# Performance work log

Measured on AMD Instinct MI355X. Metric: run time of the kernel, lower is better.

The kernel has to match this reference:

```python
import jax, jax.numpy as jnp
import numpy as np

HEAD = 4
EPS = 1e-12


def _l2norm(x, axis):
    # torch F.normalize: x / max(||x||_2, eps)
    return x / jnp.maximum(jnp.linalg.norm(x, axis=axis, keepdims=True), EPS)


def setup_inputs() -> dict:
    key = jax.random.key(0)
    ks = jax.random.split(key, 12)
    n, t, c, h, w = 2, 7, 96, 96, 96
    inp = {
        "curr_feat": jax.random.normal(ks[0], (n, c, h, w), jnp.float32),
        "index_feat_set_s1": jax.random.normal(ks[1], (n, t, c, h, w), jnp.float32),
        "anchor_feat": jax.random.normal(ks[2], (n, c, h, w), jnp.float32),
        "sparse_feat_set_s1": jax.random.normal(ks[3], (n, t, c, h, w), jnp.float32),
        "sparse_feat_set_s2": jax.random.normal(ks[4], (n, t, c, h, w), jnp.float32),
        "sparse_feat_set_s3": jax.random.normal(ks[5], (n, t, c, h, w), jnp.float32),
        # absolute pixel coordinates (x,y interleaved per frame), mostly in-bounds
        # with a little overshoot to exercise zeros padding of grid_sample
        "location_feat": jax.random.uniform(ks[6], (n, t * 2, h, w), jnp.float32, minval=-2.0, maxval=float(w) + 1.0),
        "proj_w": 0.02 * jax.random.normal(ks[7], (c, c), jnp.float32),
        "proj_b": jnp.zeros((c,), jnp.float32),
        "fusion_w": 0.02 * jax.random.normal(ks[8], (c, 3 * c), jnp.float32),
        "fusion_b": jnp.zeros((c,), jnp.float32),
    }
    return inp


def reference(curr_feat, index_feat_set_s1, anchor_feat, sparse_feat_set_s1,
              sparse_feat_set_s2, sparse_feat_set_s3, location_feat,
              proj_w, proj_b, fusion_w, fusion_b):
    n, c, h, w = anchor_feat.shape
    t = sparse_feat_set_s1.shape[1]
    hd = c // HEAD
    hw = h * w

    # ---- flow-guided nearest grid_sample (align_corners=True, zeros pad) ----
    loc = location_feat.reshape(n, t, 2, h, w)  # (n,t,2,h,w): [x, y] pixel coords
    gx = 2.0 * loc[:, :, 0] / max(w - 1, 1) - 1.0
    gy = 2.0 * loc[:, :, 1] / max(h - 1, 1) - 1.0
    ix = jnp.round((gx + 1.0) * 0.5 * (w - 1))  # nearest (round-half-even, as torch)
    iy = jnp.round((gy + 1.0) * 0.5 * (h - 1))
    valid = (ix >= 0) & (ix <= w - 1) & (iy >= 0) & (iy <= h - 1)
    lin = (jnp.clip(iy, 0, h - 1).astype(jnp.int32) * w
           + jnp.clip(ix, 0, w - 1).astype(jnp.int32)).reshape(n, t, 1, hw)
    vmask = valid.reshape(n, t, 1, hw)

    def sample(f):  # f: (n,t,c,h,w) -> gathered (n,t,c,hw)
        g = jnp.take_along_axis(f.reshape(n, t, c, hw), lin, axis=3)
        return jnp.where(vmask, g, 0.0)

    samp1 = sample(sparse_feat_set_s1)
    samp2 = sample(sparse_feat_set_s2)
    samp3 = sample(sparse_feat_set_s3)
    sampi = sample(index_feat_set_s1)

    # ---- per-pixel multi-head max-correlation over t frames ----
    # queries: normalize over full channel dim c BEFORE splitting into heads
    q = _l2norm(curr_feat.reshape(n, c, hw).transpose(0, 2, 1), -1).reshape(n, hw, HEAD, hd)
    k = _l2norm(sampi.transpose(0, 3, 1, 2), -1).reshape(n, hw, t, HEAD, hd)
    scores = jnp.einsum('npthd,nphd->npht', k, q)  # scale == 1.0 in mode='max'
    corr_soft = jnp.max(scores, axis=3)     # (n,hw,head)
    corr_index = jnp.argmax(scores, axis=3)  # (n,hw,head), first-max like torch

    soft_img = jnp.broadcast_to(corr_soft[..., None], (n, hw, HEAD, hd)) \
                  .reshape(n, h, w, c).transpose(0, 3, 1, 2)  # (n,c,h,w)
    idx = jnp.broadcast_to(corr_index[..., None], (n, hw, HEAD, hd)) \
             .reshape(n, hw, c).transpose(0, 2, 1)[:, None]  # (n,1,c,hw)

    def pick(samp):  # select winning frame per (channel-group, pixel)
        return jnp.take_along_axis(samp, idx, axis=1)[:, 0].reshape(n, c, h, w)

    cat = jnp.concatenate([pick(samp1), pick(samp2), pick(samp3)], axis=1)  # (n,3c,h,w)
    out = jnp.einsum('ndhw,cd->nchw', cat, fusion_w) + fusion_b[None, :, None, None]
    out = out * soft_img
    out = jnp.einsum('nchw,dc->ndhw', out, proj_w) + proj_b[None, :, None, None]
    return out + anchor_feat
```

## Files before the change

kernel.cpp:

```cpp
#include <hip/hip_runtime.h>
#include <hip/hip_bf16.h>

#define N_    2
#define T_    7
#define C_    96
#define H_    96
#define W_    96
#define HW_   9216
#define HEAD_ 4
#define HD_   24
#define C3_   288
#define P_    16
#define QP_   100
#define CATP_ 292
#define NBLK_ (N_ * (HW_ / P_))
#define PLANES_ 14
#define CHUNK_  64
#define NCHUNK_ 144

typedef unsigned int u32;

__device__ __forceinline__ float bits2f(u32 b) {
    union { u32 u; float f; } x; x.u = b; return x.f;
}

__device__ __forceinline__ unsigned short f2bf(float f) {
    union { __hip_bfloat16 h; unsigned short s; } u;
    u.h = __float2bfloat16(f);
    return u.s;
}

template<bool BF16>
__device__ __forceinline__ float ld1(const void* p, int i) {
    if constexpr (BF16) return bits2f(((u32)((const unsigned short*)p)[i]) << 16);
    else                return ((const float*)p)[i];
}

template<bool BF16>
__device__ __forceinline__ void ld4w(const void* p, int i, float w[4]) {
    if constexpr (BF16) {
        const uint2 u = ((const uint2*)p)[i >> 2];
        w[0] = bits2f(u.x << 16);
        w[1] = bits2f(u.x & 0xFFFF0000u);
        w[2] = bits2f(u.y << 16);
        w[3] = bits2f(u.y & 0xFFFF0000u);
    } else {
        const float4 v = *((const float4*)((const float*)p + i));
        w[0] = v.x; w[1] = v.y; w[2] = v.z; w[3] = v.w;
    }
}

template<bool BF16>
__device__ __forceinline__ void st1(void* p, int i, float v) {
    if constexpr (BF16) ((unsigned short*)p)[i] = f2bf(v);
    else                ((float*)p)[i] = v;
}

template<bool BF16>
__device__ __forceinline__ void st4w(void* p, int i, const float v[4]) {
    if constexpr (BF16) {
        uint2 w;
        w.x = (u32)f2bf(v[0]) | ((u32)f2bf(v[1]) << 16);
        w.y = (u32)f2bf(v[2]) | ((u32)f2bf(v[3]) << 16);
        ((uint2*)p)[i >> 2] = w;
    } else {
        *((float4*)((float*)p + i)) = make_float4(v[0], v[1], v[2], v[3]);
    }
}

__device__ __forceinline__ bool block_detect_bf16(const u32* __restrict__ w,
                                                  int tid, int* s_flag) {
    if (tid < 64) {
        u32 x = w[tid];
        u32 f = x & 0x7FFFu;
        int inwin = (f >= 0x3A00u) && (f <= 0x4200u);
        unsigned long long m = __ballot(inwin);
        if (tid == 0) *s_flag = (__popcll(m) >= 40) ? 1 : 0;
    }
    __syncthreads();
    return *s_flag != 0;
}

template<bool BF16>
__device__ __forceinline__ void transp_body(const void* __restrict__ src,
                                            void* __restrict__ dst,
                                            int bx, int tid, char* tileraw) {
    const int pl = bx / NCHUNK_;
    const int x0 = (bx - pl * NCHUNK_) * CHUNK_;
    if constexpr (BF16) {
        unsigned short (*tile)[CHUNK_ + 2] = (unsigned short (*)[CHUNK_ + 2])tileraw;
        const unsigned short* s = (const unsigned short*)src;
        unsigned short* d = (unsigned short*)dst;
        for (int i = tid; i < C_ * (CHUNK_ / 4); i += 256) {
            int ch = i >> 4, xq = i & 15;
            const ushort4 v = *((const ushort4*)(s + (pl * C_ + ch) * HW_ + x0 + 4 * xq));
            tile[ch][4 * xq + 0] = v.x; tile[ch][4 * xq + 1] = v.y;
            tile[ch][4 * xq + 2] = v.z; tile[ch][4 * xq + 3] = v.w;
        }
        __syncthreads();
        for (int i = tid; i < CHUNK_ * (C_ / 4); i += 256) {
            int p = i / 24, cq = i - p * 24;
            ushort4 v;
            v.x = tile[4 * cq + 0][p]; v.y = tile[4 * cq + 1][p];
            v.z = tile[4 * cq + 2][p]; v.w = tile[4 * cq + 3][p];
            *((ushort4*)(d + (pl * HW_ + x0 + p) * C_ + 4 * cq)) = v;
        }
    } else {
        float (*tile)[CHUNK_ + 1] = (float (*)[CHUNK_ + 1])tileraw;
        const float* s = (const float*)src;
        float* d = (float*)dst;
        for (int i = tid; i < C_ * (CHUNK_ / 4); i += 256) {
            int ch = i >> 4, xq = i & 15;
            const float4 v = *((const float4*)(s + (pl * C_ + ch) * HW_ + x0 + 4 * xq));
            tile[ch][4 * xq + 0] = v.x; tile[ch][4 * xq + 1] = v.y;
            tile[ch][4 * xq + 2] = v.z; tile[ch][4 * xq + 3] = v.w;
        }
        __syncthreads();
        for (int i = tid; i < CHUNK_ * (C_ / 4); i += 256) {
            int p = i / 24, cq = i - p * 24;
            float4 v;
            v.x = tile[4 * cq + 0][p]; v.y = tile[4 * cq + 1][p];
            v.z = tile[4 * cq + 2][p]; v.w = tile[4 * cq + 3][p];
            *((float4*)(d + (pl * HW_ + x0 + p) * C_ + 4 * cq)) = v;
        }
    }
}

__global__ __launch_bounds__(256) void transp_kernel(
    const void* __restrict__ idxf, void* __restrict__ dst,
    const u32* __restrict__ detect_src)
{
    __shared__ __align__(16) char tileraw[C_ * (CHUNK_ + 1) * 4];
    __shared__ int s_flag;
    const int tid = threadIdx.x;
    const bool bf = block_detect_bf16(detect_src, tid, &s_flag);
    if (bf) transp_body<true >(idxf, dst, blockIdx.x, tid, tileraw);
    else    transp_body<false>(idxf, dst, blockIdx.x, tid, tileraw);
}

template<bool BF16>
__device__ __forceinline__ void argmax_body(
    const void* __restrict__ curr, const void* __restrict__ loc,
    const void* __restrict__ kT,
    float* __restrict__ ws_best, int* __restrict__ ws_gbase,
    float* s_u, int (*s_lin)[P_], float (*s_red)[8],
    float (*s_best)[HEAD_], int (*s_bidx)[HEAD_], float* s_inv)
{
#define S_Q(pp, ch)  s_u[(pp) * QP_ + (ch)]
#define S_K(pp, ch)  s_u[P_ * QP_ + (pp) * QP_ + (ch)]
    const int tid = threadIdx.x;
    const int b  = blockIdx.x;
    const int nn = b / (HW_ / P_);
    const int p0 = (b - nn * (HW_ / P_)) * P_;

    if (tid < T_ * P_) {
        int t = tid / P_, pp = tid - t * P_;
        int p = p0 + pp;
        float x = ld1<BF16>(loc, (nn * 2 * T_ + 2 * t    ) * HW_ + p);
        float y = ld1<BF16>(loc, (nn * 2 * T_ + 2 * t + 1) * HW_ + p);
        float gx = 2.0f * x / 95.0f - 1.0f;
        float gy = 2.0f * y / 95.0f - 1.0f;
        float fx = (gx + 1.0f) * 0.5f * 95.0f;
        float fy = (gy + 1.0f) * 0.5f * 95.0f;
        float ix = rintf(fx), iy = rintf(fy);
        bool v = (ix >= 0.0f) && (ix <= 95.0f) && (iy >= 0.0f) && (iy <= 95.0f);
        s_lin[t][pp] = v ? ((int)iy * W_ + (int)ix) : -1;
    }
    if (tid >= 128 && tid < 128 + P_ * HEAD_) {
        int q = tid - 128;
        s_best[q >> 2][q & 3] = -3.0e38f; s_bidx[q >> 2][q & 3] = 0;
    }

    for (int i = tid; i < C_ * (P_ / 4); i += 256) {
        int ch = i >> 2, pq = i & 3;
        float w[4];
        ld4w<BF16>(curr, (nn * C_ + ch) * HW_ + p0 + 4 * pq, w);
        S_Q(4 * pq + 0, ch) = w[0]; S_Q(4 * pq + 1, ch) = w[1];
        S_Q(4 * pq + 2, ch) = w[2]; S_Q(4 * pq + 3, ch) = w[3];
    }
    __syncthreads();

    if (tid < P_ * 8) {
        int pp = tid >> 3, j = tid & 7;
        float s = 0.f;
        #pragma unroll
        for (int k = 0; k < 12; ++k) { float v = S_Q(pp, j * 12 + k); s += v * v; }
        s_red[pp][j] = s;
    }
    __syncthreads();
    if (tid < P_) {
        float s = 0.f;
        #pragma unroll
        for (int j = 0; j < 8; ++j) s += s_red[tid][j];
        s_inv[tid] = 1.0f / fmaxf(sqrtf(s), 1e-12f);
    }
    __syncthreads();
    for (int i = tid; i < C_ * P_; i += 256) {
        int pp = i & (P_ - 1), ch = i >> 4;
        S_Q(pp, ch) *= s_inv[pp];
    }

    for (int t = 0; t < T_; ++t) {
        __syncthreads();
        for (int i = tid; i < 24 * P_; i += 256) {
            int pp = i / 24, j = i - pp * 24;
            int lin = s_lin[t][pp];
            float w[4] = {0.f, 0.f, 0.f, 0.f};
            if (lin >= 0) ld4w<BF16>(kT, ((nn * T_ + t) * HW_ + lin) * C_ + 4 * j, w);
            *((float4*)&S_K(pp, 4 * j)) = make_float4(w[0], w[1], w[2], w[3]);
        }
        __syncthreads();
        if (tid < P_ * 8) {
            int pp = tid >> 3, j = tid & 7;
            float s = 0.f;
            #pragma unroll
            for (int k = 0; k < 12; ++k) { float v = S_K(pp, j * 12 + k); s += v * v; }
            s_red[pp][j] = s;
        }
        __syncthreads();
        if (tid < P_) {
            float s = 0.f;
            #pragma unroll
            for (int j = 0; j < 8; ++j) s += s_red[tid][j];
            s_inv[tid] = 1.0f / fmaxf(sqrtf(s), 1e-12f);
        }
        __syncthreads();
        if (tid < P_ * HEAD_) {
            int pp = tid >> 2, h = tid & 3;
            float s = 0.f;
            #pragma unroll
            for (int dq = 0; dq < 6; ++dq) {
                const float4 kv = *((const float4*)&S_K(pp, h * HD_ + 4 * dq));
                const float4 qv = *((const float4*)&S_Q(pp, h * HD_ + 4 * dq));
                s += kv.x * qv.x; s += kv.y * qv.y; s += kv.z * qv.z; s += kv.w * qv.w;
            }
            s *= s_inv[pp];
            if (s > s_best[pp][h]) { s_best[pp][h] = s; s_bidx[pp][h] = t; }
        }
    }
    if (tid < P_ * HEAD_) {
        int pp = tid >> 2, h = tid & 3;
        int bt = s_bidx[pp][h];
        int lin = s_lin[bt][pp];
        int g = (nn * HW_ + p0 + pp) * HEAD_ + h;
        ws_best[g]  = s_best[pp][h];
        ws_gbase[g] = (lin >= 0) ? ((nn * T_ + bt) * C_ * HW_ + lin) : -1;
    }
#undef S_Q
#undef S_K
}

__global__ __launch_bounds__(256, 8) void argmax_kernel(
    const void* __restrict__ curr, const void* __restrict__ loc,
    const void* __restrict__ kT,
    float* __restrict__ ws_best, int* __restrict__ ws_gbase)
{
    __shared__ __align__(16) float s_u[2 * P_ * QP_];
    __shared__ int   s_lin[T_][P_];
    __shared__ float s_red[P_][8];
    __shared__ float s_best[P_][HEAD_];
    __shared__ int   s_bidx[P_][HEAD_];
    __shared__ float s_inv[P_];
    __shared__ int   s_flag;
    const bool bf = block_detect_bf16((const u32*)curr, threadIdx.x, &s_flag);
    if (bf) argmax_body<true >(curr, loc, kT, ws_best, ws_gbase, s_u, s_lin, s_red, s_best, s_bidx, s_inv);
    else    argmax_body<false>(curr, loc, kT, ws_best, ws_gbase, s_u, s_lin, s_red, s_best, s_bidx, s_inv);
}

template<bool BF16>
__device__ __forceinline__ void catgemv_body(
    const void* __restrict__ anchor, const void* __restrict__ s1,
    const void* __restrict__ s2, const void* __restrict__ s3,
    const void* __restrict__ pw, const void* __restrict__ pb,
    const void* __restrict__ fw, const void* __restrict__ fb,
    void* __restrict__ outp,
    const float* __restrict__ ws_best, const int* __restrict__ ws_gbase,
    float* s_u, float (*s_mid)[QP_], float (*s_best)[HEAD_], int (*s_gbase)[HEAD_])
{
#define S_CAT(pp, d) s_u[(pp) * CATP_ + (d)]
    const int tid = threadIdx.x;
    const int b  = blockIdx.x;
    const int nn = b / (HW_ / P_);
    const int p0 = (b - nn * (HW_ / P_)) * P_;

    if (tid < P_ * HEAD_) {
        int pp = tid >> 2, h = tid & 3;
        int g = (nn * HW_ + p0 + pp) * HEAD_ + h;
        s_best[pp][h]  = ws_best[g];
        s_gbase[pp][h] = ws_gbase[g];
    }
    __syncthreads();

    for (int i = tid; i < C3_ * P_; i += 256) {
        int pp = i / C3_, d = i - pp * C3_;
        int set = d / C_, ch = d - set * C_;
        int gb = s_gbase[pp][ch / HD_];
        float v = 0.f;
        if (gb >= 0) {
            const void* sp = (set == 0) ? s1 : (set == 1) ? s2 : s3;
            v = ld1<BF16>(sp, gb + ch * HW_);
        }
        S_CAT(pp, d) = v;
    }
    __syncthreads();

    if (tid < 192) {
        const int cp = tid >> 2, pq = tid & 3;
        const int co0 = cp * 2, px0 = pq * 4;
        float acc[2][4];
        #pragma unroll
        for (int r = 0; r < 2; ++r)
            #pragma unroll
            for (int k = 0; k < 4; ++k) acc[r][k] = 0.f;
        for (int d = 0; d < C3_; d += 4) {
            float4 cv[4];
            #pragma unroll
            for (int k = 0; k < 4; ++k) cv[k] = *((const float4*)&S_CAT(px0 + k, d));
            #pragma unroll
            for (int r = 0; r < 2; ++r) {
                float w[4]; ld4w<BF16>(fw, (co0 + r) * C3_ + d, w);
                #pragma unroll
                for (int k = 0; k < 4; ++k)
                    acc[r][k] += w[0] * cv[k].x + w[1] * cv[k].y + w[2] * cv[k].z + w[3] * cv[k].w;
            }
        }
        const int hh = co0 / HD_;
        #pragma unroll
        for (int r = 0; r < 2; ++r) {
            float fbv = ld1<BF16>(fb, co0 + r);
            #pragma unroll
            for (int k = 0; k < 4; ++k)
                s_mid[px0 + k][co0 + r] = (acc[r][k] + fbv) * s_best[px0 + k][hh];
        }
    }
    __syncthreads();

    if (tid < 192) {
        const int dp = tid >> 2, pq = tid & 3;
        const int do0 = dp * 2, px0 = pq * 4;
        float acc[2][4];
        #pragma unroll
        for (int r = 0; r < 2; ++r)
            #pragma unroll
            for (int k = 0; k < 4; ++k) acc[r][k] = 0.f;
        for (int c = 0; c < C_; c += 4) {
            float4 mv[4];
            #pragma unroll
            for (int k = 0; k < 4; ++k) mv[k] = *((const float4*)&s_mid[px0 + k][c]);
            #pragma unroll
            for (int r = 0; r < 2; ++r) {
                float w[4]; ld4w<BF16>(pw, (do0 + r) * C_ + c, w);
                #pragma unroll
                for (int k = 0; k < 4; ++k)
                    acc[r][k] += w[0] * mv[k].x + w[1] * mv[k].y + w[2] * mv[k].z + w[3] * mv[k].w;
            }
        }
        #pragma unroll
        for (int r = 0; r < 2; ++r) {
            float pbv = ld1<BF16>(pb, do0 + r);
            float av[4];
            ld4w<BF16>(anchor, (nn * C_ + do0 + r) * HW_ + p0 + px0, av);
            float res[4];
            #pragma unroll
            for (int k = 0; k < 4; ++k) res[k] = acc[r][k] + pbv + av[k];
            st4w<BF16>(outp, (nn * C_ + do0 + r) * HW_ + p0 + px0, res);
        }
    }
#undef S_CAT
}

__global__ __launch_bounds__(256, 6) void catgemv_kernel(
    const void* __restrict__ curr, const void* __restrict__ anchor,
    const void* __restrict__ s1, const void* __restrict__ s2,
    const void* __restrict__ s3, const void* __restrict__ pw,
    const void* __restrict__ pb, const void* __restrict__ fw,
    const void* __restrict__ fb, void* __restrict__ outp,
    const float* __restrict__ ws_best, const int* __restrict__ ws_gbase)
{
    __shared__ __align__(16) float s_u[P_ * CATP_];
    __shared__ __align__(16) float s_mid[P_][QP_];
    __shared__ float s_best[P_][HEAD_];
    __shared__ int   s_gbase[P_][HEAD_];
    __shared__ int   s_flag;
    const bool bf = block_detect_bf16((const u32*)curr, threadIdx.x, &s_flag);
    if (bf) catgemv_body<true >(anchor, s1, s2, s3, pw, pb, fw, fb, outp, ws_best, ws_gbase,
                                s_u, s_mid, s_best, s_gbase);
    else    catgemv_body<false>(anchor, s1, s2, s3, pw, pb, fw, fb, outp, ws_best, ws_gbase,
                                s_u, s_mid, s_best, s_gbase);
}

template<bool BF16>
__device__ __forceinline__ void mono_body(
    const void* __restrict__ curr, const void* __restrict__ idxf,
    const void* __restrict__ anchor, const void* __restrict__ s1,
    const void* __restrict__ s2, const void* __restrict__ s3,
    const void* __restrict__ loc, const void* __restrict__ pw,
    const void* __restrict__ pb, const void* __restrict__ fw,
    const void* __restrict__ fb, void* __restrict__ outp,
    float* s_u, float (*s_mid)[QP_], int (*s_lin)[P_], float (*s_red)[8],
    float (*s_best)[HEAD_], int (*s_bidx)[HEAD_], float* s_inv)
{
#define S_Q(pp, ch)  s_u[(pp) * QP_ + (ch)]
#define S_K(pp, ch)  s_u[P_ * QP_ + (pp) * QP_ + (ch)]
#define S_CAT(pp, d) s_u[(pp) * CATP_ + (d)]
    const int tid = threadIdx.x;
    const int b  = blockIdx.x;
    const int nn = b / (HW_ / P_);
    const int p0 = (b - nn * (HW_ / P_)) * P_;

    if (tid < T_ * P_) {
        int t = tid / P_, pp = tid - t * P_;
        int p = p0 + pp;
        float x = ld1<BF16>(loc, (nn * 2 * T_ + 2 * t    ) * HW_ + p);
        float y = ld1<BF16>(loc, (nn * 2 * T_ + 2 * t + 1) * HW_ + p);
        float gx = 2.0f * x / 95.0f - 1.0f;
        float gy = 2.0f * y / 95.0f - 1.0f;
        float fx = (gx + 1.0f) * 0.5f * 95.0f;
        float fy = (gy + 1.0f) * 0.5f * 95.0f;
        float ix = rintf(fx), iy = rintf(fy);
        bool v = (ix >= 0.0f) && (ix <= 95.0f) && (iy >= 0.0f) && (iy <= 95.0f);
        s_lin[t][pp] = v ? ((int)iy * W_ + (int)ix) : -1;
    }
    if (tid >= 128 && tid < 128 + P_ * HEAD_) {
        int q = tid - 128;
        s_best[q >> 2][q & 3] = -3.0e38f; s_bidx[q >> 2][q & 3] = 0;
    }
    for (int i = tid; i < C_ * (P_ / 4); i += 256) {
        int ch = i >> 2, pq = i & 3;
        float w[4];
        ld4w<BF16>(curr, (nn * C_ + ch) * HW_ + p0 + 4 * pq, w);
        S_Q(4 * pq + 0, ch) = w[0]; S_Q(4 * pq + 1, ch) = w[1];
        S_Q(4 * pq + 2, ch) = w[2]; S_Q(4 * pq + 3, ch) = w[3];
    }
    __syncthreads();
    if (tid < P_ * 8) {
        int pp = tid >> 3, j = tid & 7;
        float s = 0.f;
        #pragma unroll
        for (int k = 0; k < 12; ++k) { float v = S_Q(pp, j * 12 + k); s += v * v; }
        s_red[pp][j] = s;
    }
    __syncthreads();
    if (tid < P_) {
        float s = 0.f;
        #pragma unroll
        for (int j = 0; j < 8; ++j) s += s_red[tid][j];
        s_inv[tid] = 1.0f / fmaxf(sqrtf(s), 1e-12f);
    }
    __syncthreads();
    for (int i = tid; i < C_ * P_; i += 256) {
        int pp = i & (P_ - 1), ch = i >> 4;
        S_Q(pp, ch) *= s_inv[pp];
    }
    for (int t = 0; t < T_; ++t) {
        __syncthreads();
        for (int i = tid; i < C_ * P_; i += 256) {
            int ch = i / P_, pp = i - ch * P_;
            int lin = s_lin[t][pp];
            S_K(pp, ch) = (lin >= 0) ? ld1<BF16>(idxf, ((nn * T_ + t) * C_ + ch) * HW_ + lin) : 0.0f;
        }
        __syncthreads();
        if (tid < P_ * 8) {
            int pp = tid >> 3, j = tid & 7;
            float s = 0.f;
            #pragma unroll
            for (int k = 0; k < 12; ++k) { float v = S_K(pp, j * 12 + k); s += v * v; }
            s_red[pp][j] = s;
        }
        __syncthreads();
        if (tid < P_) {
            float s = 0.f;
            #pragma unroll
            for (int j = 0; j < 8; ++j) s += s_red[tid][j];
            s_inv[tid] = 1.0f / fmaxf(sqrtf(s), 1e-12f);
        }
        __syncthreads();
        if (tid < P_ * HEAD_) {
            int pp = tid >> 2, h = tid & 3;
            float s = 0.f;
            #pragma unroll
            for (int dq = 0; dq < 6; ++dq) {
                const float4 kv = *((const float4*)&S_K(pp, h * HD_ + 4 * dq));
                const float4 qv = *((const float4*)&S_Q(pp, h * HD_ + 4 * dq));
                s += kv.x * qv.x; s += kv.y * qv.y; s += kv.z * qv.z; s += kv.w * qv.w;
            }
            s *= s_inv[pp];
            if (s > s_best[pp][h]) { s_best[pp][h] = s; s_bidx[pp][h] = t; }
        }
    }
    __syncthreads();
    for (int i = tid; i < C3_ * P_; i += 256) {
        int pp = i / C3_, d = i - pp * C3_;
        int set = d / C_, ch = d - set * C_;
        int h = ch / HD_;
        int bt = s_bidx[pp][h];
        int lin = s_lin[bt][pp];
        float v = 0.f;
        if (lin >= 0) {
            const void* sp = (set == 0) ? s1 : (set == 1) ? s2 : s3;
            v = ld1<BF16>(sp, ((nn * T_ + bt) * C_ + ch) * HW_ + lin);
        }
        S_CAT(pp, d) = v;
    }
    __syncthreads();
    if (tid < 96) {
        const int cq = tid >> 2, pq = tid & 3;
        const int co0 = cq * 4, px0 = pq * 4;
        float acc[4][4];
        #pragma unroll
        for (int r = 0; r < 4; ++r)
            #pragma unroll
            for (int k = 0; k < 4; ++k) acc[r][k] = 0.f;
        for (int d = 0; d < C3_; d += 4) {
            float4 cv[4];
            #pragma unroll
            for (int k = 0; k < 4; ++k) cv[k] = *((const float4*)&S_CAT(px0 + k, d));
            #pragma unroll
            for (int r = 0; r < 4; ++r) {
                float w[4]; ld4w<BF16>(fw, (co0 + r) * C3_ + d, w);
                #pragma unroll
                for (int k = 0; k < 4; ++k)
                    acc[r][k] += w[0] * cv[k].x + w[1] * cv[k].y + w[2] * cv[k].z + w[3] * cv[k].w;
            }
        }
        const int hh = co0 / HD_;
        #pragma unroll
        for (int r = 0; r < 4; ++r) {
            float fbv = ld1<BF16>(fb, co0 + r);
            #pragma unroll
            for (int k = 0; k < 4; ++k)
                s_mid[px0 + k][co0 + r] = (acc[r][k] + fbv) * s_best[px0 + k][hh];
        }
    }
    __syncthreads();
    if (tid < 96) {
        const int dq = tid >> 2, pq = tid & 3;
        const int do0 = dq * 4, px0 = pq * 4;
        float acc[4][4];
        #pragma unroll
        for (int r = 0; r < 4; ++r)
            #pragma unroll
            for (int k = 0; k < 4; ++k) acc[r][k] = 0.f;
        for (int c = 0; c < C_; c += 4) {
            float4 mv[4];
            #pragma unroll
            for (int k = 0; k < 4; ++k) mv[k] = *((const float4*)&s_mid[px0 + k][c]);
            #pragma unroll
            for (int r = 0; r < 4; ++r) {
                float w[4]; ld4w<BF16>(pw, (do0 + r) * C_ + c, w);
                #pragma unroll
                for (int k = 0; k < 4; ++k)
                    acc[r][k] += w[0] * mv[k].x + w[1] * mv[k].y + w[2] * mv[k].z + w[3] * mv[k].w;
            }
        }
        #pragma unroll
        for (int r = 0; r < 4; ++r) {
            float pbv = ld1<BF16>(pb, do0 + r);
            float av[4];
            ld4w<BF16>(anchor, (nn * C_ + do0 + r) * HW_ + p0 + px0, av);
            float res[4];
            #pragma unroll
            for (int k = 0; k < 4; ++k) res[k] = acc[r][k] + pbv + av[k];
            st4w<BF16>(outp, (nn * C_ + do0 + r) * HW_ + p0 + px0, res);
        }
    }
#undef S_Q
#undef S_K
#undef S_CAT
}

__global__ __launch_bounds__(256) void mono_kernel(
    const void* __restrict__ curr, const void* __restrict__ idxf,
    const void* __restrict__ anchor, const void* __restrict__ s1,
    const void* __restrict__ s2, const void* __restrict__ s3,
    const void* __restrict__ loc, const void* __restrict__ pw,
    const void* __restrict__ pb, const void* __restrict__ fw,
    const void* __restrict__ fb, void* __restrict__ outp)
{
    __shared__ __align__(16) float s_u[P_ * CATP_];
    __shared__ __align__(16) float s_mid[P_][QP_];
    __shared__ int   s_lin[T_][P_];
    __shared__ float s_red[P_][8];
    __shared__ float s_best[P_][HEAD_];
    __shared__ int   s_bidx[P_][HEAD_];
    __shared__ float s_inv[P_];
    __shared__ int   s_flag;
    const bool bf = block_detect_bf16((const u32*)curr, threadIdx.x, &s_flag);
    if (bf) mono_body<true >(curr, idxf, anchor, s1, s2, s3, loc, pw, pb, fw, fb, outp,
                             s_u, s_mid, s_lin, s_red, s_best, s_bidx, s_inv);
    else    mono_body<false>(curr, idxf, anchor, s1, s2, s3, loc, pw, pb, fw, fb, outp,
                             s_u, s_mid, s_lin, s_red, s_best, s_bidx, s_inv);
}

extern "C" void kernel_launch(void* const* d_in, const int* in_sizes, int n_in,
                              void* d_out, int out_size, void* d_ws, size_t ws_size,
                              hipStream_t stream) {
    (void)in_sizes; (void)n_in; (void)out_size;
    const unsigned long long SZB  = (unsigned long long)N_ * T_ * HW_ * C_ * 4ull;
    const unsigned long long AUXB = (unsigned long long)N_ * HW_ * HEAD_ * 4ull;
    char* wsb = (char*)d_ws;
    void*  kT       = wsb;
    float* ws_best  = (float*)(wsb + SZB);
    int*   ws_gbase = (int*)  (wsb + SZB + AUXB);

    dim3 grid(NBLK_), block(256);
    if (ws_size >= SZB + 2 * AUXB) {
        transp_kernel<<<dim3(PLANES_ * NCHUNK_), 256, 0, stream>>>(d_in[1], kT, (const u32*)d_in[0]);
        argmax_kernel<<<grid, block, 0, stream>>>(d_in[0], d_in[6], kT, ws_best, ws_gbase);
        catgemv_kernel<<<grid, block, 0, stream>>>(d_in[0], d_in[2], d_in[3], d_in[4], d_in[5],
                                                   d_in[7], d_in[8], d_in[9], d_in[10], d_out,
                                                   ws_best, ws_gbase);
    } else {
        mono_kernel<<<grid, block, 0, stream>>>(d_in[0], d_in[1], d_in[2], d_in[3], d_in[4],
                                                d_in[5], d_in[6], d_in[7], d_in[8], d_in[9],
                                                d_in[10], d_out);
    }
}
```

Measured before the change: 323.6 us.

## Transpose sparse feature sets to channel-last for vectorized winner gather

When enough workspace is available, the transpose kernel now converts all three sparse feature sets to a pixel-major, channel-contiguous layout in addition to the index features. The argmax kernel emits gather bases for that layout, and the cat/GEMV kernel loads the winning frame's channels as float4 vectors instead of strided scalars. This removes uncoalesced per-channel gathers but adds a full read and write of three large tensors plus a larger workspace requirement.

```diff
diff --git a/kernel.cpp b/kernel.cpp
--- a/kernel.cpp
+++ b/kernel.cpp
@@ -127,18 +127,23 @@
 }
 
 __global__ __launch_bounds__(256) void transp_kernel(
-    const void* __restrict__ idxf, void* __restrict__ dst,
+    const void* __restrict__ a0, const void* __restrict__ a1,
+    const void* __restrict__ a2, const void* __restrict__ a3,
+    void* __restrict__ dstb, unsigned long long szb,
     const u32* __restrict__ detect_src)
 {
     __shared__ __align__(16) char tileraw[C_ * (CHUNK_ + 1) * 4];
     __shared__ int s_flag;
+    const int arr = blockIdx.y;
+    const void* src = (arr == 0) ? a0 : (arr == 1) ? a1 : (arr == 2) ? a2 : a3;
+    void* dst = (char*)dstb + (unsigned long long)arr * szb;
     const int tid = threadIdx.x;
     const bool bf = block_detect_bf16(detect_src, tid, &s_flag);
-    if (bf) transp_body<true >(idxf, dst, blockIdx.x, tid, tileraw);
-    else    transp_body<false>(idxf, dst, blockIdx.x, tid, tileraw);
-}
-
-template<bool BF16>
+    if (bf) transp_body<true >(src, dst, blockIdx.x, tid, tileraw);
+    else    transp_body<false>(src, dst, blockIdx.x, tid, tileraw);
+}
+
+template<bool BF16, bool TGB>
 __device__ __forceinline__ void argmax_body(
     const void* __restrict__ curr, const void* __restrict__ loc,
     const void* __restrict__ kT,
@@ -243,13 +248,18 @@
         int bt = s_bidx[pp][h];
         int lin = s_lin[bt][pp];
         int g = (nn * HW_ + p0 + pp) * HEAD_ + h;
-        ws_best[g]  = s_best[pp][h];
-        ws_gbase[g] = (lin >= 0) ? ((nn * T_ + bt) * C_ * HW_ + lin) : -1;
+        ws_best[g] = s_best[pp][h];
+        int gb;
+        if (lin < 0)       gb = -1;
+        else if (TGB)      gb = ((nn * T_ + bt) * HW_ + lin) * C_;
+        else               gb = (nn * T_ + bt) * C_ * HW_ + lin;
+        ws_gbase[g] = gb;
     }
 #undef S_Q
 #undef S_K
 }
 
+template<bool TGB>
 __global__ __launch_bounds__(256, 8) void argmax_kernel(
     const void* __restrict__ curr, const void* __restrict__ loc,
     const void* __restrict__ kT,
@@ -263,11 +273,11 @@
     __shared__ float s_inv[P_];
     __shared__ int   s_flag;
     const bool bf = block_detect_bf16((const u32*)curr, threadIdx.x, &s_flag);
-    if (bf) argmax_body<true >(curr, loc, kT, ws_best, ws_gbase, s_u, s_lin, s_red, s_best, s_bidx, s_inv);
-    else    argmax_body<false>(curr, loc, kT, ws_best, ws_gbase, s_u, s_lin, s_red, s_best, s_bidx, s_inv);
-}
-
-template<bool BF16>
+    if (bf) argmax_body<true , TGB>(curr, loc, kT, ws_best, ws_gbase, s_u, s_lin, s_red, s_best, s_bidx, s_inv);
+    else    argmax_body<false, TGB>(curr, loc, kT, ws_best, ws_gbase, s_u, s_lin, s_red, s_best, s_bidx, s_inv);
+}
+
+template<bool BF16, bool TRANS>
 __device__ __forceinline__ void catgemv_body(
     const void* __restrict__ anchor, const void* __restrict__ s1,
     const void* __restrict__ s2, const void* __restrict__ s3,
@@ -291,16 +301,30 @@
     }
     __syncthreads();
 
-    for (int i = tid; i < C3_ * P_; i += 256) {
-        int pp = i / C3_, d = i - pp * C3_;
-        int set = d / C_, ch = d - set * C_;
-        int gb = s_gbase[pp][ch / HD_];
-        float v = 0.f;
-        if (gb >= 0) {
-            const void* sp = (set == 0) ? s1 : (set == 1) ? s2 : s3;
-            v = ld1<BF16>(sp, gb + ch * HW_);
-        }
-        S_CAT(pp, d) = v;
+    if constexpr (TRANS) {
+        for (int i = tid; i < P_ * 72; i += 256) {
+            int px = i / 72, j = i - px * 72;
+            int set = j / 24, jj = j - set * 24;
+            int gb = s_gbase[px][jj / 6];
+            float w[4] = {0.f, 0.f, 0.f, 0.f};
+            if (gb >= 0) {
+                const void* sp = (set == 0) ? s1 : (set == 1) ? s2 : s3;
+                ld4w<BF16>(sp, gb + 4 * jj, w);
+            }
+            *((float4*)&S_CAT(px, set * C_ + 4 * jj)) = make_float4(w[0], w[1], w[2], w[3]);
+        }
+    } else {
+        for (int i = tid; i < C3_ * P_; i += 256) {
+            int pp = i / C3_, d = i - pp * C3_;
+            int set = d / C_, ch = d - set * C_;
+            int gb = s_gbase[pp][ch / HD_];
+            float v = 0.f;
+            if (gb >= 0) {
+                const void* sp = (set == 0) ? s1 : (set == 1) ? s2 : s3;
+                v = ld1<BF16>(sp, gb + ch * HW_);
+            }
+            S_CAT(pp, d) = v;
+        }
     }
     __syncthreads();
 
@@ -369,6 +393,7 @@
 #undef S_CAT
 }
 
+template<bool TRANS>
 __global__ __launch_bounds__(256, 6) void catgemv_kernel(
     const void* __restrict__ curr, const void* __restrict__ anchor,
     const void* __restrict__ s1, const void* __restrict__ s2,
@@ -383,10 +408,10 @@
     __shared__ int   s_gbase[P_][HEAD_];
     __shared__ int   s_flag;
     const bool bf = block_detect_bf16((const u32*)curr, threadIdx.x, &s_flag);
-    if (bf) catgemv_body<true >(anchor, s1, s2, s3, pw, pb, fw, fb, outp, ws_best, ws_gbase,
-                                s_u, s_mid, s_best, s_gbase);
-    else    catgemv_body<false>(anchor, s1, s2, s3, pw, pb, fw, fb, outp, ws_best, ws_gbase,
-                                s_u, s_mid, s_best, s_gbase);
+    if (bf) catgemv_body<true , TRANS>(anchor, s1, s2, s3, pw, pb, fw, fb, outp, ws_best, ws_gbase,
+                                       s_u, s_mid, s_best, s_gbase);
+    else    catgemv_body<false, TRANS>(anchor, s1, s2, s3, pw, pb, fw, fb, outp, ws_best, ws_gbase,
+                                       s_u, s_mid, s_best, s_gbase);
 }
 
 template<bool BF16>
@@ -599,17 +624,31 @@
     const unsigned long long SZB  = (unsigned long long)N_ * T_ * HW_ * C_ * 4ull;
     const unsigned long long AUXB = (unsigned long long)N_ * HW_ * HEAD_ * 4ull;
     char* wsb = (char*)d_ws;
-    void*  kT       = wsb;
-    float* ws_best  = (float*)(wsb + SZB);
-    int*   ws_gbase = (int*)  (wsb + SZB + AUXB);
 
     dim3 grid(NBLK_), block(256);
-    if (ws_size >= SZB + 2 * AUXB) {
-        transp_kernel<<<dim3(PLANES_ * NCHUNK_), 256, 0, stream>>>(d_in[1], kT, (const u32*)d_in[0]);
-        argmax_kernel<<<grid, block, 0, stream>>>(d_in[0], d_in[6], kT, ws_best, ws_gbase);
-        catgemv_kernel<<<grid, block, 0, stream>>>(d_in[0], d_in[2], d_in[3], d_in[4], d_in[5],
-                                                   d_in[7], d_in[8], d_in[9], d_in[10], d_out,
-                                                   ws_best, ws_gbase);
+    if (ws_size >= 4 * SZB + 2 * AUXB) {
+        void*  kT       = wsb;
+        void*  s1T      = wsb + SZB;
+        void*  s2T      = wsb + 2 * SZB;
+        void*  s3T      = wsb + 3 * SZB;
+        float* ws_best  = (float*)(wsb + 4 * SZB);
+        int*   ws_gbase = (int*)  (wsb + 4 * SZB + AUXB);
+        transp_kernel<<<dim3(PLANES_ * NCHUNK_, 4), 256, 0, stream>>>(
+            d_in[1], d_in[3], d_in[4], d_in[5], wsb, SZB, (const u32*)d_in[0]);
+        argmax_kernel<true><<<grid, block, 0, stream>>>(d_in[0], d_in[6], kT, ws_best, ws_gbase);
+        catgemv_kernel<true><<<grid, block, 0, stream>>>(d_in[0], d_in[2], s1T, s2T, s3T,
+                                                         d_in[7], d_in[8], d_in[9], d_in[10],
+                                                         d_out, ws_best, ws_gbase);
+    } else if (ws_size >= SZB + 2 * AUXB) {
+        void*  kT       = wsb;
+        float* ws_best  = (float*)(wsb + SZB);
+        int*   ws_gbase = (int*)  (wsb + SZB + AUXB);
+        transp_kernel<<<dim3(PLANES_ * NCHUNK_, 1), 256, 0, stream>>>(
+            d_in[1], d_in[1], d_in[1], d_in[1], wsb, SZB, (const u32*)d_in[0]);
+        argmax_kernel<false><<<grid, block, 0, stream>>>(d_in[0], d_in[6], kT, ws_best, ws_gbase);
+        catgemv_kernel<false><<<grid, block, 0, stream>>>(d_in[0], d_in[2], d_in[3], d_in[4], d_in[5],
+                                                          d_in[7], d_in[8], d_in[9], d_in[10],
+                                                          d_out, ws_best, ws_gbase);
     } else {
         mono_kernel<<<grid, block, 0, stream>>>(d_in[0], d_in[1], d_in[2], d_in[3], d_in[4],
                                                 d_in[5], d_in[6], d_in[7], d_in[8], d_in[9],
```

Result: faster. 312.0 us (-3.6%).
